# Kernel tuning notes

Measured on AMD Instinct MI355X. Metric: run time of the kernel, lower is better.

The kernel has to match this reference:

```python
import jax, jax.numpy as jnp
import numpy as np

EMBED = 1024
HEADS = 16
HEAD = EMBED // HEADS
B, S = 8, 1024


def setup_inputs() -> dict:
    key = jax.random.key(0)
    ks = jax.random.split(key, 12)
    inp = {
        "values": jax.random.normal(ks[0], (B, S, EMBED), jnp.float32),
        "keys": jax.random.normal(ks[1], (B, S, EMBED), jnp.float32),
        "query": jax.random.normal(ks[2], (B, S, EMBED), jnp.float32),
        # causal mask broadcastable to [B, heads, q, k]
        "mask": jnp.broadcast_to(jnp.tril(jnp.ones((S, S), jnp.int32))[None, None], (B, 1, S, S)),
        "Wv": jax.random.normal(ks[3], (HEAD, HEAD), jnp.float32) / np.sqrt(HEAD),
        "bv": jnp.zeros((HEAD,), jnp.float32),
        "Wk": jax.random.normal(ks[4], (HEAD, HEAD), jnp.float32) / np.sqrt(HEAD),
        "bk": jnp.zeros((HEAD,), jnp.float32),
        "Wq": jax.random.normal(ks[5], (HEAD, HEAD), jnp.float32) / np.sqrt(HEAD),
        "bq": jnp.zeros((HEAD,), jnp.float32),
        "Wfc": jax.random.normal(ks[6], (EMBED, EMBED), jnp.float32) / np.sqrt(EMBED),
        "bfc": jnp.zeros((EMBED,), jnp.float32),
    }
    return inp


def reference(values, keys, query, mask, Wv, bv, Wk, bk, Wq, bq, Wfc, bfc):
    N, q_len = query.shape[0], query.shape[1]
    k_len, v_len = keys.shape[1], values.shape[1]
    # split heads: [N, S, H, D]
    v = values.reshape(N, v_len, HEADS, HEAD)
    k = keys.reshape(N, k_len, HEADS, HEAD)
    q = query.reshape(N, q_len, HEADS, HEAD)
    # per-head linear projections (torch Linear: x @ W.T + b)
    v = v @ Wv.T + bv
    k = k @ Wk.T + bk
    q = q @ Wq.T + bq
    # scores [N, H, q, k]
    scores = jnp.einsum('nqhz,nkhz->nhqk', q, k)
    scores = jnp.where(mask == 0, -jnp.inf, scores)
    # NOTE: original divides by sqrt(query_size) (sequence length), not head dim
    attn = jax.nn.softmax(scores / jnp.sqrt(jnp.float32(q_len)), axis=-1)
    out = jnp.einsum('nhqk,nkhz->nqhz', attn, v).reshape(N, q_len, HEADS * HEAD)
    return out @ Wfc.T + bfc
```

## Files before the change

kernel.cpp:

```cpp
#include <hip/hip_runtime.h>
#include <stdint.h>

typedef __attribute__((ext_vector_type(8))) short short8;
typedef __attribute__((ext_vector_type(4))) short short4v;
typedef __attribute__((ext_vector_type(4))) float floatx4;
typedef __attribute__((ext_vector_type(4))) unsigned short ushort4v;

#define HEADS 16
#define HEAD 64
#define SEQ 1024
#define BATCH 8

__device__ __forceinline__ unsigned short f2bf(float f) {
    union { float f; unsigned int u; } v; v.f = f;
    unsigned int r = v.u + 0x7FFFu + ((v.u >> 16) & 1u);
    return (unsigned short)(r >> 16);
}

__device__ __forceinline__ void gload_lds16(const void* g, void* l) {
    __builtin_amdgcn_global_load_lds((const __attribute__((address_space(1))) void*)g,
                                     (__attribute__((address_space(3))) void*)l, 16, 0, 0);
}

__global__ __launch_bounds__(256) void cvt_kernel(const float* __restrict__ in,
                                                  unsigned short* __restrict__ out) {
    int i = (blockIdx.x * 256 + threadIdx.x) * 4;
    float4 f = *(const float4*)(in + i);
    ushort4v v;
    v.x = f2bf(f.x); v.y = f2bf(f.y); v.z = f2bf(f.z); v.w = f2bf(f.w);
    *(ushort4v*)(out + i) = v;
}

__global__ __launch_bounds__(256) void proj_kernel(
    const float* __restrict__ Vin, const float* __restrict__ Kin, const float* __restrict__ Qin,
    const float* __restrict__ Wv, const float* __restrict__ bv,
    const float* __restrict__ Wk, const float* __restrict__ bk,
    const float* __restrict__ Wq, const float* __restrict__ bq,
    unsigned short* __restrict__ q_ws, unsigned short* __restrict__ k_ws,
    unsigned short* __restrict__ v_ws)
{
    const int tid = threadIdx.x;
    const int tile = blockIdx.x;
    const int ph = blockIdx.y;
    const int proj = ph >> 4;
    const int h = ph & 15;

    const float* X; const float* W; const float* bias;
    if (proj == 0)      { X = Qin; W = Wq; bias = bq; }
    else if (proj == 1) { X = Kin; W = Wk; bias = bk; }
    else                { X = Vin; W = Wv; bias = bv; }

    __shared__ unsigned short sW[64 * 64];
    __shared__ unsigned short sX[64 * 72];

    const int wave = tid >> 6, lane = tid & 63;
    const int lq = lane & 15, quad = lane >> 4;
    const int m0 = tile * 64;

    {
        int n = tid >> 2, c0 = (tid & 3) * 16;
        const float* wr = W + n * 64 + c0;
#pragma unroll
        for (int half = 0; half < 2; ++half) {
            float4 fa = *(const float4*)(wr + half * 8);
            float4 fb = *(const float4*)(wr + half * 8 + 4);
            short8 v;
            v[0] = (short)f2bf(fa.x); v[1] = (short)f2bf(fa.y);
            v[2] = (short)f2bf(fa.z); v[3] = (short)f2bf(fa.w);
            v[4] = (short)f2bf(fb.x); v[5] = (short)f2bf(fb.y);
            v[6] = (short)f2bf(fb.z); v[7] = (short)f2bf(fb.w);
            int chunk = ((c0 >> 3) + half) ^ (n & 7);
            *(short8*)&sW[n * 64 + chunk * 8] = v;
        }
    }

    short8 afr[2];
    {
        const float* xr = X + (size_t)(m0 + wave * 16 + lq) * 1024 + h * 64;
#pragma unroll
        for (int ks = 0; ks < 2; ++ks) {
            float4 f0 = *(const float4*)(xr + quad * 8 + ks * 32);
            float4 f1 = *(const float4*)(xr + quad * 8 + ks * 32 + 4);
            short8 a;
            a[0] = (short)f2bf(f0.x); a[1] = (short)f2bf(f0.y);
            a[2] = (short)f2bf(f0.z); a[3] = (short)f2bf(f0.w);
            a[4] = (short)f2bf(f1.x); a[5] = (short)f2bf(f1.y);
            a[6] = (short)f2bf(f1.z); a[7] = (short)f2bf(f1.w);
            afr[ks] = a;
        }
    }
    __syncthreads();

    const floatx4 zero4 = {0.f, 0.f, 0.f, 0.f};
    floatx4 acc[4] = {zero4, zero4, zero4, zero4};
#pragma unroll
    for (int ks = 0; ks < 2; ++ks) {
#pragma unroll
        for (int nt = 0; nt < 4; ++nt) {
            int n = nt * 16 + lq;
            short8 bfr = *(const short8*)&sW[n * 64 + (((quad + 4 * ks) ^ (n & 7)) * 8)];
            acc[nt] = __builtin_amdgcn_mfma_f32_16x16x32_bf16(afr[ks], bfr, acc[nt], 0, 0, 0);
        }
    }

    const float qscale = 0.03125f * 1.44269504088896340736f;
#pragma unroll
    for (int nt = 0; nt < 4; ++nt) {
        int d = nt * 16 + lq;
        float bcol = bias[d];
#pragma unroll
        for (int r = 0; r < 4; ++r) {
            int srow = wave * 16 + quad * 4 + r;
            float ov = acc[nt][r] + bcol;
            if (proj == 0) ov *= qscale;
            sX[srow * 72 + d] = f2bf(ov);
        }
    }
    __syncthreads();

    const int b = m0 >> 10, s0 = m0 & 1023;
    if (proj < 2) {
        unsigned short* dstb = (proj == 0 ? q_ws : k_ws);
        int r = tid >> 2, c = (tid & 3) * 16;
        unsigned short* dst = dstb + ((size_t)((b * 16 + h) * 1024 + s0 + r)) * 64 + c;
        const unsigned short* src = sX + r * 72 + c;
        ((short4v*)dst)[0] = *(const short4v*)(src);
        ((short4v*)dst)[1] = *(const short4v*)(src + 4);
        ((short4v*)dst)[2] = *(const short4v*)(src + 8);
        ((short4v*)dst)[3] = *(const short4v*)(src + 12);
    } else {
        int d = tid >> 2, c = (tid & 3) * 16;
        short8 v0, v1;
#pragma unroll
        for (int j = 0; j < 8; ++j) v0[j] = (short)sX[(c + j) * 72 + d];
#pragma unroll
        for (int j = 0; j < 8; ++j) v1[j] = (short)sX[(c + 8 + j) * 72 + d];
        unsigned short* dst = v_ws + ((size_t)((b * 16 + h) * 64 + d)) * 1024 + s0 + c;
        *(short8*)dst = v0;
        *(short8*)(dst + 8) = v1;
    }
}

__global__ __launch_bounds__(256, 2) void attn_kernel(
    const unsigned short* __restrict__ q_ws, const unsigned short* __restrict__ k_ws,
    const unsigned short* __restrict__ v_ws, unsigned short* __restrict__ attn_ws)
{
    const int bh = blockIdx.x;
    const int b = bh >> 4, h = bh & 15;
    const int tid = threadIdx.x;
    const int wave = tid >> 6, lane = tid & 63;
    const int lq = lane & 15, quad = lane >> 4;
    const int r8 = lane >> 3, ch = lane & 7;
    const int sw = ch ^ r8;

    __shared__ unsigned short sK[64 * 64];
    __shared__ unsigned short sV[64 * 64];
    __shared__ unsigned short sP[4][32 * 64];

    const size_t head_off = (size_t)bh * SEQ * HEAD;
    const unsigned short* qb = q_ws + head_off;
    const unsigned short* kb = k_ws + head_off;
    const unsigned short* vb = v_ws + head_off;

    short8 ones;
#pragma unroll
    for (int j = 0; j < 8; ++j) ones[j] = (short)0x3F80;

    const floatx4 zero4 = {0.f, 0.f, 0.f, 0.f};

    for (int pass = 0; pass < 2; ++pass) {
        const int qt = pass ? (7 - blockIdx.y) : blockIdx.y;
        const int q0 = qt * 128;
        const int q_lo = q0 + wave * 32;
        const int q_hi = q_lo + 31;
        const int nkt = 2 * qt + 2;

        short8 aq[2][2];
#pragma unroll
        for (int rg = 0; rg < 2; ++rg) {
            const unsigned short* qp = qb + (size_t)(q0 + wave * 32 + rg * 16 + lq) * 64 + quad * 8;
            aq[rg][0] = *(const short8*)qp;
            aq[rg][1] = *(const short8*)(qp + 32);
        }

        floatx4 o[2][4];
        floatx4 lacc[2] = {zero4, zero4};
#pragma unroll
        for (int rg = 0; rg < 2; ++rg)
#pragma unroll
            for (int nt = 0; nt < 4; ++nt) o[rg][nt] = zero4;

        for (int kt = 0; kt < nkt; ++kt) {
#pragma unroll
            for (int i = 0; i < 2; ++i) {
                int br = wave * 16 + i * 8;
                const char* gK = (const char*)(kb + (size_t)(kt * 64 + br + r8) * 64) + sw * 16;
                gload_lds16(gK, (char*)sK + br * 128);
                const char* gV = (const char*)(vb + (size_t)(br + r8) * 1024 + kt * 64) + sw * 16;
                gload_lds16(gV, (char*)sV + br * 128);
            }
            __syncthreads();

            const bool skip = (kt * 64 > q_hi);
            if (!skip) {
                const bool full = (kt * 64 + 63 <= q_lo);

                floatx4 s[2][4];
#pragma unroll
                for (int rg = 0; rg < 2; ++rg)
#pragma unroll
                    for (int nt = 0; nt < 4; ++nt) s[rg][nt] = zero4;
#pragma unroll
                for (int ks = 0; ks < 2; ++ks) {
#pragma unroll
                    for (int nt = 0; nt < 4; ++nt) {
                        short8 kf = *(const short8*)(sK + (nt * 16 + lq) * 64 +
                                                     (((quad + 4 * ks) ^ (lq & 7)) * 8));
                        s[0][nt] = __builtin_amdgcn_mfma_f32_16x16x32_bf16(aq[0][ks], kf, s[0][nt], 0, 0, 0);
                        s[1][nt] = __builtin_amdgcn_mfma_f32_16x16x32_bf16(aq[1][ks], kf, s[1][nt], 0, 0, 0);
                    }
                }

                unsigned short* wp = &sP[wave][0];
#pragma unroll
                for (int rg = 0; rg < 2; ++rg) {
#pragma unroll
                    for (int nt = 0; nt < 4; ++nt) {
                        int kcol = kt * 64 + nt * 16 + lq;
                        int chn = (((nt * 2 + (lq >> 3)) ^ (quad << 1)) * 8) + (lq & 7);
#pragma unroll
                        for (int r = 0; r < 4; ++r) {
                            float p = __builtin_amdgcn_exp2f(s[rg][nt][r]);
                            if (!full) {
                                int qrow = q_lo + rg * 16 + quad * 4 + r;
                                if (kcol > qrow) p = 0.f;
                            }
                            wp[(rg * 16 + quad * 4 + r) * 64 + chn] = f2bf(p);
                        }
                    }
                }

                short8 vf[4][2];
#pragma unroll
                for (int nt = 0; nt < 4; ++nt)
#pragma unroll
                    for (int ks = 0; ks < 2; ++ks)
                        vf[nt][ks] = *(const short8*)(sV + (nt * 16 + lq) * 64 +
                                                      (((quad + 4 * ks) ^ (lq & 7)) * 8));
#pragma unroll
                for (int rg = 0; rg < 2; ++rg) {
#pragma unroll
                    for (int ks = 0; ks < 2; ++ks) {
                        short8 pa = *(const short8*)&sP[wave][(rg * 16 + lq) * 64 +
                                     (((ks * 4 + quad) ^ (((lq >> 2) & 3) << 1)) * 8)];
                        lacc[rg] = __builtin_amdgcn_mfma_f32_16x16x32_bf16(pa, ones, lacc[rg], 0, 0, 0);
#pragma unroll
                        for (int nt = 0; nt < 4; ++nt)
                            o[rg][nt] = __builtin_amdgcn_mfma_f32_16x16x32_bf16(pa, vf[nt][ks], o[rg][nt], 0, 0, 0);
                    }
                }
            }
            __syncthreads();
        }

#pragma unroll
        for (int rg = 0; rg < 2; ++rg) {
            float inv[4];
#pragma unroll
            for (int r = 0; r < 4; ++r) inv[r] = 1.f / lacc[rg][r];
            const int srow_base = q0 + wave * 32 + rg * 16 + quad * 4;
#pragma unroll
            for (int nt = 0; nt < 4; ++nt) {
                int col = h * 64 + nt * 16 + lq;
#pragma unroll
                for (int r = 0; r < 4; ++r) {
                    attn_ws[((size_t)(b * SEQ + srow_base + r)) * 1024 + col] = f2bf(o[rg][nt][r] * inv[r]);
                }
            }
        }
    }
}

__global__ __launch_bounds__(256) void fc_kernel(
    const unsigned short* __restrict__ A, const unsigned short* __restrict__ Bw,
    const float* __restrict__ bias, float* __restrict__ out)
{
    const int nt0 = blockIdx.x * 128;
    const int mt0 = blockIdx.y * 128;
    const int tid = threadIdx.x;
    const int wave = tid >> 6, lane = tid & 63;
    const int lq = lane & 15, quad = lane >> 4;
    const int wm = (wave >> 1) * 64, wn = (wave & 1) * 64;

    __shared__ unsigned short sA[128 * 32];
    __shared__ unsigned short sB[128 * 32];

    const floatx4 zero4 = {0.f, 0.f, 0.f, 0.f};
    floatx4 acc[4][4];
#pragma unroll
    for (int i = 0; i < 4; ++i)
#pragma unroll
        for (int j = 0; j < 4; ++j) acc[i][j] = zero4;

    for (int kt = 0; kt < 32; ++kt) {
#pragma unroll
        for (int issue = 0; issue < 2; ++issue) {
            int off = (issue * 4 + wave) * 1024 + lane * 16;
            int row = off >> 6;
            int cb = off & 63;
            const char* ga = (const char*)A + (size_t)(mt0 + row) * 2048 + kt * 64 + cb;
            gload_lds16(ga, (char*)sA + (issue * 4 + wave) * 1024);
            const char* gb = (const char*)Bw + (size_t)(nt0 + row) * 2048 + kt * 64 + cb;
            gload_lds16(gb, (char*)sB + (issue * 4 + wave) * 1024);
        }
        __syncthreads();

        short8 af[4], bf[4];
#pragma unroll
        for (int i = 0; i < 4; ++i) {
            af[i] = *(const short8*)(sA + (wm + i * 16 + lq) * 32 + quad * 8);
            bf[i] = *(const short8*)(sB + (wn + i * 16 + lq) * 32 + quad * 8);
        }
#pragma unroll
        for (int mi = 0; mi < 4; ++mi)
#pragma unroll
            for (int ni = 0; ni < 4; ++ni)
                acc[mi][ni] = __builtin_amdgcn_mfma_f32_16x16x32_bf16(af[mi], bf[ni], acc[mi][ni], 0, 0, 0);
        __syncthreads();
    }

#pragma unroll
    for (int mi = 0; mi < 4; ++mi) {
#pragma unroll
        for (int ni = 0; ni < 4; ++ni) {
            int col = nt0 + wn + ni * 16 + lq;
            float bc = bias[col];
#pragma unroll
            for (int r = 0; r < 4; ++r) {
                int row = mt0 + wm + mi * 16 + quad * 4 + r;
                out[(size_t)row * 1024 + col] = acc[mi][ni][r] + bc;
            }
        }
    }
}

extern "C" void kernel_launch(void* const* d_in, const int* in_sizes, int n_in,
                              void* d_out, int out_size, void* d_ws, size_t ws_size,
                              hipStream_t stream)
{
    const float* values = (const float*)d_in[0];
    const float* keys   = (const float*)d_in[1];
    const float* query  = (const float*)d_in[2];
    const float* Wv  = (const float*)d_in[4];
    const float* bv  = (const float*)d_in[5];
    const float* Wk  = (const float*)d_in[6];
    const float* bk  = (const float*)d_in[7];
    const float* Wq  = (const float*)d_in[8];
    const float* bq  = (const float*)d_in[9];
    const float* Wfc = (const float*)d_in[10];
    const float* bfc = (const float*)d_in[11];
    float* out = (float*)d_out;

    char* ws = (char*)d_ws;
    unsigned short* q_ws    = (unsigned short*)(ws);
    unsigned short* k_ws    = (unsigned short*)(ws + (16u << 20));
    unsigned short* v_ws    = (unsigned short*)(ws + (32u << 20));
    unsigned short* attn_ws = (unsigned short*)(ws + (48u << 20));
    unsigned short* wfc_ws  = (unsigned short*)(ws + (64u << 20));

    cvt_kernel<<<dim3(1024), dim3(256), 0, stream>>>(Wfc, wfc_ws);
    proj_kernel<<<dim3(128, 48), dim3(256), 0, stream>>>(
        values, keys, query, Wv, bv, Wk, bk, Wq, bq, q_ws, k_ws, v_ws);
    attn_kernel<<<dim3(128, 4), dim3(256), 0, stream>>>(q_ws, k_ws, v_ws, attn_ws);
    fc_kernel<<<dim3(8, 64), dim3(256), 0, stream>>>(attn_ws, wfc_ws, bfc, out);
}
```

Before: 246.4 us.

## Restructure projection per-wave heads and transpose score MFMA for vectorized P stores

The projection kernel now launches one block per 32 rows per projection. Each block loads the shared 64x64 weight once, and each wave loops over four heads, so the weight is converted and staged far less often. The Q scale is folded into the weights and bias. The attention kernel computes scores transposed (K as the A operand), which lets each lane pack four probabilities into one short4 LDS store with a new swizzle instead of scalar stores. Launch bounds are raised to 3 blocks per CU, which may add register pressure or spills.

Measured after the change: 252.8 us. +2.6%, slower.

```diff
diff --git a/kernel.cpp b/kernel.cpp
--- a/kernel.cpp
+++ b/kernel.cpp
@@ -31,7 +31,7 @@
     *(ushort4v*)(out + i) = v;
 }
 
-__global__ __launch_bounds__(256) void proj_kernel(
+__global__ __launch_bounds__(256, 3) void proj_kernel(
     const float* __restrict__ Vin, const float* __restrict__ Kin, const float* __restrict__ Qin,
     const float* __restrict__ Wv, const float* __restrict__ bv,
     const float* __restrict__ Wk, const float* __restrict__ bk,
@@ -41,9 +41,7 @@
 {
     const int tid = threadIdx.x;
     const int tile = blockIdx.x;
-    const int ph = blockIdx.y;
-    const int proj = ph >> 4;
-    const int h = ph & 15;
+    const int proj = blockIdx.y;
 
     const float* X; const float* W; const float* bias;
     if (proj == 0)      { X = Qin; W = Wq; bias = bq; }
@@ -51,11 +49,15 @@
     else                { X = Vin; W = Wv; bias = bv; }
 
     __shared__ unsigned short sW[64 * 64];
-    __shared__ unsigned short sX[64 * 72];
+    __shared__ unsigned short sE[4][32 * 72];
 
     const int wave = tid >> 6, lane = tid & 63;
     const int lq = lane & 15, quad = lane >> 4;
-    const int m0 = tile * 64;
+    const int m0 = tile * 32;
+    const int b = m0 >> 10, s0 = m0 & 1023;
+
+    const float qscale = 0.03125f * 1.44269504088896340736f;
+    const float wscale = (proj == 0) ? qscale : 1.0f;
 
     {
         int n = tid >> 2, c0 = (tid & 3) * 16;
@@ -65,83 +67,100 @@
             float4 fa = *(const float4*)(wr + half * 8);
             float4 fb = *(const float4*)(wr + half * 8 + 4);
             short8 v;
-            v[0] = (short)f2bf(fa.x); v[1] = (short)f2bf(fa.y);
-            v[2] = (short)f2bf(fa.z); v[3] = (short)f2bf(fa.w);
-            v[4] = (short)f2bf(fb.x); v[5] = (short)f2bf(fb.y);
-            v[6] = (short)f2bf(fb.z); v[7] = (short)f2bf(fb.w);
+            v[0] = (short)f2bf(fa.x * wscale); v[1] = (short)f2bf(fa.y * wscale);
+            v[2] = (short)f2bf(fa.z * wscale); v[3] = (short)f2bf(fa.w * wscale);
+            v[4] = (short)f2bf(fb.x * wscale); v[5] = (short)f2bf(fb.y * wscale);
+            v[6] = (short)f2bf(fb.z * wscale); v[7] = (short)f2bf(fb.w * wscale);
             int chunk = ((c0 >> 3) + half) ^ (n & 7);
             *(short8*)&sW[n * 64 + chunk * 8] = v;
         }
     }
 
-    short8 afr[2];
-    {
-        const float* xr = X + (size_t)(m0 + wave * 16 + lq) * 1024 + h * 64;
-#pragma unroll
-        for (int ks = 0; ks < 2; ++ks) {
-            float4 f0 = *(const float4*)(xr + quad * 8 + ks * 32);
-            float4 f1 = *(const float4*)(xr + quad * 8 + ks * 32 + 4);
-            short8 a;
-            a[0] = (short)f2bf(f0.x); a[1] = (short)f2bf(f0.y);
-            a[2] = (short)f2bf(f0.z); a[3] = (short)f2bf(f0.w);
-            a[4] = (short)f2bf(f1.x); a[5] = (short)f2bf(f1.y);
-            a[6] = (short)f2bf(f1.z); a[7] = (short)f2bf(f1.w);
-            afr[ks] = a;
-        }
-    }
+    float biasv[4];
+#pragma unroll
+    for (int nt = 0; nt < 4; ++nt) biasv[nt] = bias[nt * 16 + lq] * wscale;
+
     __syncthreads();
 
-    const floatx4 zero4 = {0.f, 0.f, 0.f, 0.f};
-    floatx4 acc[4] = {zero4, zero4, zero4, zero4};
-#pragma unroll
-    for (int ks = 0; ks < 2; ++ks) {
+    short8 bfr[2][4];
+#pragma unroll
+    for (int ks = 0; ks < 2; ++ks)
 #pragma unroll
         for (int nt = 0; nt < 4; ++nt) {
             int n = nt * 16 + lq;
-            short8 bfr = *(const short8*)&sW[n * 64 + (((quad + 4 * ks) ^ (n & 7)) * 8)];
-            acc[nt] = __builtin_amdgcn_mfma_f32_16x16x32_bf16(afr[ks], bfr, acc[nt], 0, 0, 0);
-        }
-    }
-
-    const float qscale = 0.03125f * 1.44269504088896340736f;
-#pragma unroll
-    for (int nt = 0; nt < 4; ++nt) {
-        int d = nt * 16 + lq;
-        float bcol = bias[d];
-#pragma unroll
-        for (int r = 0; r < 4; ++r) {
-            int srow = wave * 16 + quad * 4 + r;
-            float ov = acc[nt][r] + bcol;
-            if (proj == 0) ov *= qscale;
-            sX[srow * 72 + d] = f2bf(ov);
-        }
-    }
-    __syncthreads();
-
-    const int b = m0 >> 10, s0 = m0 & 1023;
-    if (proj < 2) {
-        unsigned short* dstb = (proj == 0 ? q_ws : k_ws);
-        int r = tid >> 2, c = (tid & 3) * 16;
-        unsigned short* dst = dstb + ((size_t)((b * 16 + h) * 1024 + s0 + r)) * 64 + c;
-        const unsigned short* src = sX + r * 72 + c;
-        ((short4v*)dst)[0] = *(const short4v*)(src);
-        ((short4v*)dst)[1] = *(const short4v*)(src + 4);
-        ((short4v*)dst)[2] = *(const short4v*)(src + 8);
-        ((short4v*)dst)[3] = *(const short4v*)(src + 12);
-    } else {
-        int d = tid >> 2, c = (tid & 3) * 16;
-        short8 v0, v1;
-#pragma unroll
-        for (int j = 0; j < 8; ++j) v0[j] = (short)sX[(c + j) * 72 + d];
-#pragma unroll
-        for (int j = 0; j < 8; ++j) v1[j] = (short)sX[(c + 8 + j) * 72 + d];
-        unsigned short* dst = v_ws + ((size_t)((b * 16 + h) * 64 + d)) * 1024 + s0 + c;
-        *(short8*)dst = v0;
-        *(short8*)(dst + 8) = v1;
-    }
-}
-
-__global__ __launch_bounds__(256, 2) void attn_kernel(
+            bfr[ks][nt] = *(const short8*)&sW[n * 64 + (((quad + 4 * ks) ^ (n & 7)) * 8)];
+        }
+
+    const floatx4 zero4 = {0.f, 0.f, 0.f, 0.f};
+
+    for (int hh = 0; hh < 4; ++hh) {
+        const int h = wave * 4 + hh;
+
+        short8 afr[2][2];
+#pragma unroll
+        for (int rg = 0; rg < 2; ++rg) {
+            const float* xr = X + (size_t)(m0 + rg * 16 + lq) * 1024 + h * 64;
+#pragma unroll
+            for (int ks = 0; ks < 2; ++ks) {
+                float4 f0 = *(const float4*)(xr + quad * 8 + ks * 32);
+                float4 f1 = *(const float4*)(xr + quad * 8 + ks * 32 + 4);
+                short8 a;
+                a[0] = (short)f2bf(f0.x); a[1] = (short)f2bf(f0.y);
+                a[2] = (short)f2bf(f0.z); a[3] = (short)f2bf(f0.w);
+                a[4] = (short)f2bf(f1.x); a[5] = (short)f2bf(f1.y);
+                a[6] = (short)f2bf(f1.z); a[7] = (short)f2bf(f1.w);
+                afr[rg][ks] = a;
+            }
+        }
+
+        floatx4 acc[2][4];
+#pragma unroll
+        for (int rg = 0; rg < 2; ++rg)
+#pragma unroll
+            for (int nt = 0; nt < 4; ++nt) acc[rg][nt] = zero4;
+#pragma unroll
+        for (int ks = 0; ks < 2; ++ks)
+#pragma unroll
+            for (int nt = 0; nt < 4; ++nt) {
+                acc[0][nt] = __builtin_amdgcn_mfma_f32_16x16x32_bf16(afr[0][ks], bfr[ks][nt], acc[0][nt], 0, 0, 0);
+                acc[1][nt] = __builtin_amdgcn_mfma_f32_16x16x32_bf16(afr[1][ks], bfr[ks][nt], acc[1][nt], 0, 0, 0);
+            }
+
+#pragma unroll
+        for (int rg = 0; rg < 2; ++rg)
+#pragma unroll
+            for (int nt = 0; nt < 4; ++nt)
+#pragma unroll
+                for (int r = 0; r < 4; ++r)
+                    sE[wave][(rg * 16 + quad * 4 + r) * 72 + nt * 16 + lq] =
+                        f2bf(acc[rg][nt][r] + biasv[nt]);
+
+        if (proj < 2) {
+            unsigned short* dstb = (proj == 0 ? q_ws : k_ws);
+#pragma unroll
+            for (int r2 = 0; r2 < 2; ++r2) {
+                int row = r2 * 16 + (lane >> 2), c = (lane & 3) * 16;
+                const unsigned short* src = &sE[wave][row * 72 + c];
+                unsigned short* dst = dstb + ((size_t)((b * 16 + h) * 1024 + s0 + row)) * 64 + c;
+                *(short8*)dst = *(const short8*)src;
+                *(short8*)(dst + 8) = *(const short8*)(src + 8);
+            }
+        } else {
+            int d = lane;
+            short8 v[4];
+#pragma unroll
+            for (int g = 0; g < 4; ++g)
+#pragma unroll
+                for (int j = 0; j < 8; ++j)
+                    v[g][j] = (short)sE[wave][(g * 8 + j) * 72 + d];
+            unsigned short* dst = v_ws + ((size_t)((b * 16 + h) * 64 + d)) * 1024 + s0;
+#pragma unroll
+            for (int g = 0; g < 4; ++g) *(short8*)(dst + g * 8) = v[g];
+        }
+    }
+}
+
+__global__ __launch_bounds__(256, 3) void attn_kernel(
     const unsigned short* __restrict__ q_ws, const unsigned short* __restrict__ k_ws,
     const unsigned short* __restrict__ v_ws, unsigned short* __restrict__ attn_ws)
 {
@@ -205,38 +224,38 @@
             if (!skip) {
                 const bool full = (kt * 64 + 63 <= q_lo);
 
-                floatx4 s[2][4];
+                floatx4 sT[2][4];
 #pragma unroll
                 for (int rg = 0; rg < 2; ++rg)
 #pragma unroll
-                    for (int nt = 0; nt < 4; ++nt) s[rg][nt] = zero4;
+                    for (int nt = 0; nt < 4; ++nt) sT[rg][nt] = zero4;
 #pragma unroll
                 for (int ks = 0; ks < 2; ++ks) {
 #pragma unroll
                     for (int nt = 0; nt < 4; ++nt) {
                         short8 kf = *(const short8*)(sK + (nt * 16 + lq) * 64 +
                                                      (((quad + 4 * ks) ^ (lq & 7)) * 8));
-                        s[0][nt] = __builtin_amdgcn_mfma_f32_16x16x32_bf16(aq[0][ks], kf, s[0][nt], 0, 0, 0);
-                        s[1][nt] = __builtin_amdgcn_mfma_f32_16x16x32_bf16(aq[1][ks], kf, s[1][nt], 0, 0, 0);
+                        sT[0][nt] = __builtin_amdgcn_mfma_f32_16x16x32_bf16(kf, aq[0][ks], sT[0][nt], 0, 0, 0);
+                        sT[1][nt] = __builtin_amdgcn_mfma_f32_16x16x32_bf16(kf, aq[1][ks], sT[1][nt], 0, 0, 0);
                     }
                 }
 
                 unsigned short* wp = &sP[wave][0];
 #pragma unroll
                 for (int rg = 0; rg < 2; ++rg) {
+                    int q = q_lo + rg * 16 + lq;
 #pragma unroll
                     for (int nt = 0; nt < 4; ++nt) {
-                        int kcol = kt * 64 + nt * 16 + lq;
-                        int chn = (((nt * 2 + (lq >> 3)) ^ (quad << 1)) * 8) + (lq & 7);
+                        int kcol0 = kt * 64 + nt * 16 + quad * 4;
+                        short4v pk;
 #pragma unroll
                         for (int r = 0; r < 4; ++r) {
-                            float p = __builtin_amdgcn_exp2f(s[rg][nt][r]);
-                            if (!full) {
-                                int qrow = q_lo + rg * 16 + quad * 4 + r;
-                                if (kcol > qrow) p = 0.f;
-                            }
-                            wp[(rg * 16 + quad * 4 + r) * 64 + chn] = f2bf(p);
+                            float p = __builtin_amdgcn_exp2f(sT[rg][nt][r]);
+                            if (!full && (kcol0 + r > q)) p = 0.f;
+                            pk[r] = (short)f2bf(p);
                         }
+                        *(short4v*)&wp[(rg * 16 + lq) * 64 +
+                                       (((nt * 2 + (quad >> 1)) ^ (lq & 7)) * 8) + (quad & 1) * 4] = pk;
                     }
                 }
 
@@ -252,7 +271,7 @@
 #pragma unroll
                     for (int ks = 0; ks < 2; ++ks) {
                         short8 pa = *(const short8*)&sP[wave][(rg * 16 + lq) * 64 +
-                                     (((ks * 4 + quad) ^ (((lq >> 2) & 3) << 1)) * 8)];
+                                     (((ks * 4 + quad) ^ (lq & 7)) * 8)];
                         lacc[rg] = __builtin_amdgcn_mfma_f32_16x16x32_bf16(pa, ones, lacc[rg], 0, 0, 0);
 #pragma unroll
                         for (int nt = 0; nt < 4; ++nt)
@@ -369,7 +388,7 @@
     unsigned short* wfc_ws  = (unsigned short*)(ws + (64u << 20));
 
     cvt_kernel<<<dim3(1024), dim3(256), 0, stream>>>(Wfc, wfc_ws);
-    proj_kernel<<<dim3(128, 48), dim3(256), 0, stream>>>(
+    proj_kernel<<<dim3(256, 3), dim3(256), 0, stream>>>(
         values, keys, query, Wv, bv, Wk, bk, Wq, bq, q_ws, k_ws, v_ws);
     attn_kernel<<<dim3(128, 4), dim3(256), 0, stream>>>(q_ws, k_ws, v_ws, attn_ws);
     fc_kernel<<<dim3(8, 64), dim3(256), 0, stream>>>(attn_ws, wfc_ws, bfc, out);
```
